# Performance work log

Hardware: AMD Instinct MI355X
Metric: run time of the kernel (lower is better)

The kernel has to match this reference:

```python
import jax, jax.numpy as jnp
import numpy as np

EPS = 1e-8
NUM_ITER = 3
NUM_SLOTS = 8
NUM_HEADS = 4


def _ln(x, w, b):
    m = x.mean(-1, keepdims=True)
    v = x.var(-1, keepdims=True)
    return (x - m) / jnp.sqrt(v + 1e-5) * w + b


def setup_inputs() -> dict:
    key = jax.random.key(0)
    B, T, N, D, S, H = 16, 12, 1024, 256, 128, 256
    K = NUM_SLOTS
    ks = jax.random.split(key, 32)
    w = lambda i, shape: (0.02 * jax.random.normal(ks[i], shape)).astype(jnp.float32)
    f32 = jnp.float32
    return {
        'inputs': jax.random.normal(ks[0], (B, T, N, D), f32),
        'slots_noise': jax.random.normal(ks[1], (B, K, S), f32),
        'slot_mu': w(2, (1, 1, S)),
        'slot_log_sigma': w(3, (1, 1, S)),
        'ln_in_w': jnp.ones((D,), f32), 'ln_in_b': jnp.zeros((D,), f32),
        'ln_slots_w': jnp.ones((S,), f32), 'ln_slots_b': jnp.zeros((S,), f32),
        'ln_mlp_w': jnp.ones((S,), f32), 'ln_mlp_b': jnp.zeros((S,), f32),
        'Wq': w(4, (S, S)), 'Wk': w(5, (D, S)), 'Wv': w(6, (D, S)),
        'gru_Wih': w(7, (3 * S, S)), 'gru_Whh': w(8, (3 * S, S)),
        'gru_bih': jnp.zeros((3 * S,), f32), 'gru_bhh': jnp.zeros((3 * S,), f32),
        'mlp_W1': w(9, (S, H)), 'mlp_b1': jnp.zeros((H,), f32),
        'mlp_W2': w(10, (H, S)), 'mlp_b2': jnp.zeros((S,), f32),
        'p_ln1_w': jnp.ones((S,), f32), 'p_ln1_b': jnp.zeros((S,), f32),
        'p_Wq': w(11, (S, S)), 'p_Wk': w(12, (S, S)), 'p_Wv': w(13, (S, S)), 'p_Wo': w(14, (S, S)),
        'p_ln2_w': jnp.ones((S,), f32), 'p_ln2_b': jnp.zeros((S,), f32),
        'p_ffn_W1': w(15, (S, 4 * S)), 'p_ffn_b1': jnp.zeros((4 * S,), f32),
        'p_ffn_W2': w(16, (4 * S, S)), 'p_ffn_b2': jnp.zeros((S,), f32),
        'p_lnf_w': jnp.ones((S,), f32), 'p_lnf_b': jnp.zeros((S,), f32),
    }


def reference(inputs, slots_noise, slot_mu, slot_log_sigma,
              ln_in_w, ln_in_b, ln_slots_w, ln_slots_b, ln_mlp_w, ln_mlp_b,
              Wq, Wk, Wv, gru_Wih, gru_Whh, gru_bih, gru_bhh,
              mlp_W1, mlp_b1, mlp_W2, mlp_b2,
              p_ln1_w, p_ln1_b, p_Wq, p_Wk, p_Wv, p_Wo,
              p_ln2_w, p_ln2_b, p_ffn_W1, p_ffn_b1, p_ffn_W2, p_ffn_b2,
              p_lnf_w, p_lnf_b):
    B, T, N, D = inputs.shape
    S = slot_mu.shape[-1]
    K = NUM_SLOTS

    slots0 = slot_mu + jnp.exp(slot_log_sigma) * slots_noise  # (B,K,S)
    x = _ln(inputs, ln_in_w, ln_in_b)
    k = (x @ Wk) * (S ** -0.5)  # (B,T,N,S), pre-scaled keys
    v = x @ Wv                  # (B,T,N,S)

    def gru(u, h):  # torch GRUCell semantics; u,h: (B*K,S)
        gi = u @ gru_Wih.T + gru_bih
        gh = h @ gru_Whh.T + gru_bhh
        i_r, i_z, i_n = jnp.split(gi, 3, -1)
        h_r, h_z, h_n = jnp.split(gh, 3, -1)
        r = jax.nn.sigmoid(i_r + h_r)
        z = jax.nn.sigmoid(i_z + h_z)
        n = jnp.tanh(i_n + r * h_n)
        return (1.0 - z) * n + z * h

    def mha(y):  # (B,K,S) self-attention, pre-LN block style
        dh = S // NUM_HEADS
        split = lambda t: t.reshape(B, K, NUM_HEADS, dh).transpose(0, 2, 1, 3)
        q = split(y @ p_Wq) * (dh ** -0.5)
        kk = split(y @ p_Wk)
        vv = split(y @ p_Wv)
        a = jax.nn.softmax(jnp.einsum('bhqd,bhkd->bhqk', q, kk), -1)
        o = jnp.einsum('bhqk,bhkd->bhqd', a, vv).transpose(0, 2, 1, 3).reshape(B, K, S)
        return o @ p_Wo

    def predictor(s):
        s = s + mha(_ln(s, p_ln1_w, p_ln1_b))
        h = _ln(s, p_ln2_w, p_ln2_b)
        s = s + (jax.nn.relu(h @ p_ffn_W1 + p_ffn_b1) @ p_ffn_W2 + p_ffn_b2)
        return _ln(s, p_lnf_w, p_lnf_b)

    def step(slots, kv_t):
        k_t, v_t = kv_t  # (B,N,S) each
        attn_vis = None
        for i in range(NUM_ITER):
            slots_prev = slots
            q = _ln(slots, ln_slots_w, ln_slots_b) @ Wq          # (B,K,S)
            logits = jnp.einsum('bns,bks->bnk', k_t, q)           # (B,N,K)
            attn_vis = jax.nn.softmax(logits, -1)                 # over slots
            attn = attn_vis + EPS
            attn = attn / attn.sum(1, keepdims=True)              # normalize over inputs
            updates = jnp.einsum('bnk,bns->bks', attn, v_t)       # (B,K,S)
            slots = gru(updates.reshape(-1, S), slots_prev.reshape(-1, S)).reshape(B, K, S)
            if i < NUM_ITER - 1:
                h = _ln(slots, ln_mlp_w, ln_mlp_b)
                slots = slots + (jax.nn.relu(h @ mlp_W1 + mlp_b1) @ mlp_W2 + mlp_b2)
        return predictor(slots), (slots, attn_vis)

    kT = jnp.swapaxes(k, 0, 1)  # (T,B,N,S)
    vT = jnp.swapaxes(v, 0, 1)
    _, (slots_seq, attn_seq) = jax.lax.scan(step, slots0, (kT, vT))
    slots_collect = jnp.swapaxes(slots_seq, 0, 1)  # (B,T,K,S)
    attns_collect = jnp.swapaxes(attn_seq, 0, 1)   # (B,T,N,K)
    return slots_collect, attns_collect
```

## Files before the change

kernel.cpp:

```cpp
#include <hip/hip_runtime.h>
#include <hip/hip_bf16.h>

typedef _Float16 half8 __attribute__((ext_vector_type(8)));
typedef float floatx4 __attribute__((ext_vector_type(4)));

#define MFMA_F16(a, b, c) __builtin_amdgcn_mfma_f32_16x16x32_f16((a), (b), (c), 0, 0, 0)

struct PrepJobs {
  const float* src[11];
  _Float16* dst[11];
  int In[11], Out[11], elems[11], doT[11];
  float scale[11];
};

__global__ void prep_all_kernel(PrepJobs J) {
  int j = blockIdx.y;
  int idx = blockIdx.x * 256 + threadIdx.x;
  if (idx >= J.elems[j]) return;
  float v;
  if (J.doT[j]) { int o = idx / J.In[j], i = idx - o * J.In[j]; v = J.src[j][i * J.Out[j] + o]; }
  else          { v = J.src[j][idx]; }
  J.dst[j][idx] = (_Float16)(v * J.scale[j]);
}

__global__ void prep_wtilde_kernel(const float* __restrict__ Wk, const float* __restrict__ Wq,
                                   _Float16* __restrict__ WT, float scale) {
  int idx = blockIdx.x * 256 + threadIdx.x;
  int s = idx >> 8, i = idx & 255;
  const float* wk = Wk + (size_t)i * 128;
  const float* wq = Wq + (size_t)s * 128;
  float acc = 0.f;
  #pragma unroll 4
  for (int o = 0; o < 128; o++) acc += wk[o] * wq[o];
  WT[idx] = (_Float16)(acc * scale);
}

__global__ void init_ctr_kernel(int* __restrict__ ctr) {
  ctr[threadIdx.x] = 0;
}

__global__ __launch_bounds__(256) void gemm_kv_kernel(
    const float* __restrict__ x, const float* __restrict__ lnw_g,
    const float* __restrict__ lnb_g, const _Float16* __restrict__ WT,
    _Float16* __restrict__ kout, _Float16* __restrict__ vTout) {
  __shared__ union {
    struct { _Float16 A[128][72]; _Float16 B[128][72]; } s;
    _Float16 C[128][136];
  } u;
  __shared__ float s_mean[128], s_rstd[128], s_red[256][2], s_lnw[256], s_lnb[256];

  const int tid = threadIdx.x;
  const int bx = blockIdx.x, y = blockIdx.y;
  const size_t r0 = (size_t)bx * 128;
  const int w = tid >> 6, lane = tid & 63, quad = lane >> 4, l15 = lane & 15;

  s_lnw[tid] = lnw_g[tid];
  s_lnb[tid] = lnb_g[tid];
  {
    int row = tid >> 1, half = tid & 1;
    const float* p = x + (r0 + row) * 256 + half * 128;
    float s = 0.f, sq = 0.f;
    for (int i = 0; i < 32; i++) {
      float4 d = ((const float4*)p)[i];
      s += d.x + d.y + d.z + d.w;
      sq += d.x * d.x + d.y * d.y + d.z * d.z + d.w * d.w;
    }
    s_red[tid][0] = s; s_red[tid][1] = sq;
  }
  __syncthreads();
  if (tid < 128) {
    float s  = s_red[2 * tid][0] + s_red[2 * tid + 1][0];
    float sq = s_red[2 * tid][1] + s_red[2 * tid + 1][1];
    float m = s * (1.f / 256.f);
    float v = sq * (1.f / 256.f) - m * m;
    s_mean[tid] = m; s_rstd[tid] = rsqrtf(v + 1e-5f);
  }

  floatx4 acc[2][8];
  for (int rt = 0; rt < 2; rt++)
    for (int ct = 0; ct < 8; ct++) acc[rt][ct] = (floatx4){0.f, 0.f, 0.f, 0.f};

  for (int c = 0; c < 4; c++) {
    __syncthreads();
    for (int i = 0; i < 4; i++) {
      int g = tid + 256 * i;
      int row = g >> 3, c8 = g & 7;
      int col0 = c * 64 + c8 * 8;
      const float* p = x + (r0 + row) * 256 + col0;
      float4 d0 = ((const float4*)p)[0];
      float4 d1 = ((const float4*)p)[1];
      float f[8] = {d0.x, d0.y, d0.z, d0.w, d1.x, d1.y, d1.z, d1.w};
      float m = s_mean[row], rs = s_rstd[row];
      half8 hv;
      #pragma unroll
      for (int j = 0; j < 8; j++)
        hv[j] = (_Float16)((f[j] - m) * rs * s_lnw[col0 + j] + s_lnb[col0 + j]);
      *(half8*)&u.s.A[row][c8 * 8] = hv;
      *(half8*)&u.s.B[row][c8 * 8] = *(const half8*)(WT + (size_t)(y * 128 + row) * 256 + col0);
    }
    __syncthreads();
    #pragma unroll
    for (int ks = 0; ks < 2; ks++) {
      half8 af[2];
      af[0] = *(const half8*)&u.s.A[(2 * w) * 16 + l15][ks * 32 + quad * 8];
      af[1] = *(const half8*)&u.s.A[(2 * w + 1) * 16 + l15][ks * 32 + quad * 8];
      #pragma unroll
      for (int ct = 0; ct < 8; ct++) {
        half8 bf = *(const half8*)&u.s.B[ct * 16 + l15][ks * 32 + quad * 8];
        acc[0][ct] = MFMA_F16(af[0], bf, acc[0][ct]);
        acc[1][ct] = MFMA_F16(af[1], bf, acc[1][ct]);
      }
    }
  }

  const size_t bt = (size_t)(bx >> 3);
  const int n0loc = (bx & 7) * 128;
  if (y == 0) {
    for (int rt = 0; rt < 2; rt++)
      for (int ct = 0; ct < 8; ct++)
        #pragma unroll
        for (int r = 0; r < 4; r++) {
          size_t row = r0 + (2 * w + rt) * 16 + quad * 4 + r;
          kout[row * 128 + ct * 16 + l15] = (_Float16)acc[rt][ct][r];
        }
  } else {
    __syncthreads();
    for (int rt = 0; rt < 2; rt++)
      for (int ct = 0; ct < 8; ct++)
        #pragma unroll
        for (int r = 0; r < 4; r++)
          u.C[(2 * w + rt) * 16 + quad * 4 + r][ct * 16 + l15] = (_Float16)acc[rt][ct][r];
    __syncthreads();
    int s = tid >> 1, hf = tid & 1;
    for (int j = 0; j < 8; j++) {
      int nb = hf * 64 + j * 8;
      half8 tmp;
      #pragma unroll
      for (int e = 0; e < 8; e++) tmp[e] = u.C[nb + e][s];
      *(half8*)(vTout + (bt * 128 + s) * 1024 + n0loc + nb) = tmp;
    }
  }
}

struct P2Args {
  const _Float16 *kbuf, *vT;
  const _Float16 *Wih, *Whh, *W1T, *W2T;
  const _Float16 *pQT, *pKT, *pVT, *pOT, *pF1T, *pF2T;
  const float *noise, *mu, *lsig;
  const float *lnsw, *lnsb, *lnmw, *lnmb;
  const float *bih, *bhh, *mb1, *mb2;
  const float *pl1w, *pl1b, *pl2w, *pl2b, *fb1, *fb2, *plfw, *plfb;
  float *out_slots, *out_attn;
  float *upd_p;
  float *col_p;
  int   *ctr;
};

struct SH {
  _Float16 k_lds[128][136];
  _Float16 v_lds[128][136];
  float slots[8][128];
  _Float16 a16[16][136];
  _Float16 h16[16][136];
  float gh[8][384];
  union {
    struct { _Float16 attnT[16][136]; float wcs[16][8]; } sa;
    struct { _Float16 m16[16][264]; } mlp;
    struct { float qh[8][128]; float kh[8][128]; float vh[8][128]; float sc[4][8][8]; } mha;
    struct { _Float16 f16[16][520]; } ffn;
  } u;
  float bih[384], bhh[384], mb1[256], mb2[128], fb1[512], fb2[128];
  float lnsw[128], lnsb[128], lnmw[128], lnmb[128];
  float pl1w[128], pl1b[128], pl2w[128], pl2b[128], plfw[128], plfb[128];
};

__device__ __forceinline__ void group_barrier(int* ctr, int target) {
  __syncthreads();
  if (threadIdx.x == 0) {
    __hip_atomic_fetch_add(ctr, 1, __ATOMIC_ACQ_REL, __HIP_MEMORY_SCOPE_AGENT);
    while (__hip_atomic_load(ctr, __ATOMIC_ACQUIRE, __HIP_MEMORY_SCOPE_AGENT) < target)
      __builtin_amdgcn_s_sleep(1);
  }
  __syncthreads();
}

__device__ __forceinline__ void ln_to_a16(SH* sh, const float (*src)[128],
                                          const float* wv, const float* bv,
                                          int w, int lane) {
  if (w < 8) {
    float x0 = src[w][lane], x1 = src[w][lane + 64];
    float s = x0 + x1, sq = x0 * x0 + x1 * x1;
    #pragma unroll
    for (int m = 1; m < 64; m <<= 1) { s += __shfl_xor(s, m); sq += __shfl_xor(sq, m); }
    float mn = s * 0.0078125f;
    float vr = sq * 0.0078125f - mn * mn;
    float rs = rsqrtf(vr + 1e-5f);
    sh->a16[w][lane]      = (_Float16)((x0 - mn) * rs * wv[lane]      + bv[lane]);
    sh->a16[w][lane + 64] = (_Float16)((x1 - mn) * rs * wv[lane + 64] + bv[lane + 64]);
  }
}

__global__ __launch_bounds__(1024, 4) void slot_attn_kernel(P2Args P) {
  __shared__ SH sh;
  const int tid = threadIdx.x;
  const int w = tid >> 6, lane = tid & 63, quad = lane >> 4, l15 = lane & 15;
  const int b = blockIdx.x & 15;
  const int g = blockIdx.x >> 4;
  const int n0 = g * 128;
  int* ctrb = P.ctr + b * 64;
  int bar_phase = 0;

  for (int i = tid; i < 384; i += 1024) { sh.bih[i] = P.bih[i]; sh.bhh[i] = P.bhh[i]; }
  for (int i = tid; i < 256; i += 1024) sh.mb1[i] = P.mb1[i];
  for (int i = tid; i < 512; i += 1024) sh.fb1[i] = P.fb1[i];
  if (tid < 128) {
    sh.mb2[tid]  = P.mb2[tid];  sh.fb2[tid]  = P.fb2[tid];
    sh.lnsw[tid] = P.lnsw[tid]; sh.lnsb[tid] = P.lnsb[tid];
    sh.lnmw[tid] = P.lnmw[tid]; sh.lnmb[tid] = P.lnmb[tid];
    sh.pl1w[tid] = P.pl1w[tid]; sh.pl1b[tid] = P.pl1b[tid];
    sh.pl2w[tid] = P.pl2w[tid]; sh.pl2b[tid] = P.pl2b[tid];
    sh.plfw[tid] = P.plfw[tid]; sh.plfb[tid] = P.plfb[tid];
  }
  {
    int kk = tid >> 7, s = tid & 127;
    float v = P.mu[s] + expf(P.lsig[s]) * P.noise[(b * 8 + kk) * 128 + s];
    sh.slots[kk][s] = v;
    sh.h16[kk][s] = (_Float16)v;
  }
  if (w >= 8) {
    sh.a16[w][lane] = (_Float16)0.f; sh.a16[w][lane + 64] = (_Float16)0.f;
    sh.h16[w][lane] = (_Float16)0.f; sh.h16[w][lane + 64] = (_Float16)0.f;
  }
  __syncthreads();

  for (int t = 0; t < 12; t++) {
    const _Float16* kt = P.kbuf + ((size_t)(b * 12 + t)) * 1024 * 128 + (size_t)n0 * 128;
    const _Float16* vt = P.vT   + ((size_t)(b * 12 + t)) * 128 * 1024 + n0;
    {
      int r = tid >> 4, c8 = (tid & 15) * 8;
      #pragma unroll
      for (int p = 0; p < 2; p++) {
        int row = p * 64 + r;
        *(half8*)&sh.k_lds[row][c8] = *(const half8*)(kt + (size_t)row * 128 + c8);
        *(half8*)&sh.v_lds[row][c8] = *(const half8*)(vt + (size_t)row * 1024 + c8);
      }
    }
    __syncthreads();

    for (int it = 0; it < 3; it++) {
      const int par = (t * 3 + it) & 1;
      float* updg = P.upd_p + ((size_t)(par * 16 + b) * 8 + g) * 1152;
      float* colg = P.col_p + ((size_t)(par * 16 + b) * 8 + g) * 64;
      if (w < 8) {
        float x0 = sh.slots[w][lane], x1 = sh.slots[w][lane + 64];
        float s = x0 + x1, sq = x0 * x0 + x1 * x1;
        #pragma unroll
        for (int m = 1; m < 64; m <<= 1) { s += __shfl_xor(s, m); sq += __shfl_xor(sq, m); }
        float mn = s * 0.0078125f;
        float vr = sq * 0.0078125f - mn * mn;
        float rs = rsqrtf(vr + 1e-5f);
        sh.a16[w][lane]      = (_Float16)((x0 - mn) * rs * sh.lnsw[lane]      + sh.lnsb[lane]);
        sh.a16[w][lane + 64] = (_Float16)((x1 - mn) * rs * sh.lnsw[lane + 64] + sh.lnsb[lane + 64]);
      } else {
        const int idx8 = w - 8;
        const _Float16* ar = &sh.h16[l15][quad * 8];
        #pragma unroll
        for (int tt = 0; tt < 3; tt++) {
          int ct = idx8 + tt * 8;
          const _Float16* Bg = P.Whh + (size_t)(ct * 16 + l15) * 128 + quad * 8;
          floatx4 acc = (floatx4){0.f, 0.f, 0.f, 0.f};
          #pragma unroll
          for (int ks = 0; ks < 4; ks++)
            acc = MFMA_F16(*(const half8*)(ar + ks * 32), *(const half8*)(Bg + ks * 32), acc);
          int col = ct * 16 + l15;
          #pragma unroll
          for (int r = 0; r < 4; r++) {
            int slot = quad * 4 + r;
            if (slot < 8) sh.gh[slot][col] = acc[r] + sh.bhh[col];
          }
        }
      }
      __syncthreads();
      {
        int nloc0 = (w & 7) * 16;
        int rhalf = w >> 3;
        floatx4 acc = (floatx4){0.f, 0.f, 0.f, 0.f};
        const _Float16* ar = &sh.k_lds[nloc0 + l15][quad * 8];
        const _Float16* br = &sh.a16[l15][quad * 8];
        #pragma unroll
        for (int ks = 0; ks < 4; ks++)
          acc = MFMA_F16(*(const half8*)(ar + ks * 32), *(const half8*)(br + ks * 32), acc);
        float cs = 0.f;
        #pragma unroll
        for (int rr = 0; rr < 2; rr++) {
          int r = rhalf * 2 + rr;
          float v = (l15 < 8) ? acc[r] : -3.0e38f;
          float mx = v;
          mx = fmaxf(mx, __shfl_xor(mx, 1, 16));
          mx = fmaxf(mx, __shfl_xor(mx, 2, 16));
          mx = fmaxf(mx, __shfl_xor(mx, 4, 16));
          mx = fmaxf(mx, __shfl_xor(mx, 8, 16));
          float pv = (l15 < 8) ? expf(v - mx) : 0.f;
          float ss = pv;
          ss += __shfl_xor(ss, 1, 16); ss += __shfl_xor(ss, 2, 16);
          ss += __shfl_xor(ss, 4, 16); ss += __shfl_xor(ss, 8, 16);
          float pn = pv / ss;
          cs += pn;
          int nloc = nloc0 + quad * 4 + r;
          sh.u.sa.attnT[l15][nloc] = (l15 == 8) ? (_Float16)1.f : (_Float16)pn;
          if (it == 2 && l15 < 8)
            P.out_attn[((size_t)(b * 12 + t) * 1024 + n0 + nloc) * 8 + l15] = pn;
        }
        cs += __shfl_xor(cs, 16); cs += __shfl_xor(cs, 32);
        if (lane < 8) sh.u.sa.wcs[w][lane] = cs;
      }
      __syncthreads();
      if (w < 8) {
        floatx4 acc = (floatx4){0.f, 0.f, 0.f, 0.f};
        const _Float16* ar = &sh.u.sa.attnT[l15][quad * 8];
        const _Float16* br = &sh.v_lds[w * 16 + l15][quad * 8];
        #pragma unroll
        for (int ks = 0; ks < 4; ks++)
          acc = MFMA_F16(*(const half8*)(ar + ks * 32), *(const half8*)(br + ks * 32), acc);
        int scol = w * 16 + l15;
        #pragma unroll
        for (int r = 0; r < 4; r++) {
          int row = quad * 4 + r;
          if (row < 9)
            __hip_atomic_store(&updg[row * 128 + scol], acc[r],
                               __ATOMIC_RELAXED, __HIP_MEMORY_SCOPE_AGENT);
        }
      }
      if (tid < 8) {
        float c = 0.f;
        #pragma unroll
        for (int ww = 0; ww < 16; ww++) c += sh.u.sa.wcs[ww][tid];
        __hip_atomic_store(&colg[tid], c, __ATOMIC_RELAXED, __HIP_MEMORY_SCOPE_AGENT);
      }
      bar_phase++;
      group_barrier(ctrb, 8 * bar_phase);
      {
        int slot = tid >> 7, scol = tid & 127;
        const float* upb = P.upd_p + (size_t)(par * 16 + b) * 8 * 1152;
        float sum = 0.f, vs = 0.f;
        #pragma unroll
        for (int gg = 0; gg < 8; gg++) {
          sum += __hip_atomic_load((float*)(upb + gg * 1152 + slot * 128 + scol),
                                   __ATOMIC_RELAXED, __HIP_MEMORY_SCOPE_AGENT);
          vs  += __hip_atomic_load((float*)(upb + gg * 1152 + 8 * 128 + scol),
                                   __ATOMIC_RELAXED, __HIP_MEMORY_SCOPE_AGENT);
        }
        const float* cpb = P.col_p + (size_t)(par * 16 + b) * 8 * 64;
        float csum = 0.f;
        #pragma unroll
        for (int gg = 0; gg < 8; gg++)
          csum += __hip_atomic_load((float*)(cpb + gg * 64 + slot),
                                    __ATOMIC_RELAXED, __HIP_MEMORY_SCOPE_AGENT);
        float upd = (sum + 1e-8f * vs) / (csum + 1024.f * 1e-8f);
        sh.a16[slot][scol] = (_Float16)upd;
      }
      __syncthreads();
      if (w < 8) {
        const _Float16* ar = &sh.a16[l15][quad * 8];
        const _Float16* B0 = P.Wih + (size_t)(w * 16 + l15) * 128 + quad * 8;
        const _Float16* B1 = P.Wih + (size_t)((w + 8) * 16 + l15) * 128 + quad * 8;
        const _Float16* B2 = P.Wih + (size_t)((w + 16) * 16 + l15) * 128 + quad * 8;
        floatx4 ac = (floatx4){0.f, 0.f, 0.f, 0.f};
        floatx4 az = (floatx4){0.f, 0.f, 0.f, 0.f};
        floatx4 an = (floatx4){0.f, 0.f, 0.f, 0.f};
        #pragma unroll
        for (int ks = 0; ks < 4; ks++) {
          half8 af = *(const half8*)(ar + ks * 32);
          ac = MFMA_F16(af, *(const half8*)(B0 + ks * 32), ac);
          az = MFMA_F16(af, *(const half8*)(B1 + ks * 32), az);
          an = MFMA_F16(af, *(const half8*)(B2 + ks * 32), an);
        }
        int col = w * 16 + l15;
        #pragma unroll
        for (int r = 0; r < 4; r++) {
          int slot = quad * 4 + r;
          if (slot < 8) {
            float gic = ac[r] + sh.bih[col];
            float giz = az[r] + sh.bih[128 + col];
            float gin = an[r] + sh.bih[256 + col];
            float rg = 1.f / (1.f + expf(-(gic + sh.gh[slot][col])));
            float zg = 1.f / (1.f + expf(-(giz + sh.gh[slot][128 + col])));
            float ng = tanhf(gin + rg * sh.gh[slot][256 + col]);
            float h = sh.slots[slot][col];
            float x = (1.f - zg) * ng + zg * h;
            sh.slots[slot][col] = x;
            if (it == 2)
              P.out_slots[((size_t)(b * 12 + t) * 8 + slot) * 128 + col] = x;
          }
        }
      }
      __syncthreads();
      ln_to_a16(&sh, sh.slots, (it < 2) ? sh.lnmw : sh.pl1w,
                (it < 2) ? sh.lnmb : sh.pl1b, w, lane);
      __syncthreads();
      if (it < 2) {
        {
          floatx4 acc = (floatx4){0.f, 0.f, 0.f, 0.f};
          const _Float16* ar = &sh.a16[l15][quad * 8];
          const _Float16* br = P.W1T + (size_t)(w * 16 + l15) * 128 + quad * 8;
          #pragma unroll
          for (int ks = 0; ks < 4; ks++)
            acc = MFMA_F16(*(const half8*)(ar + ks * 32), *(const half8*)(br + ks * 32), acc);
          int col = w * 16 + l15;
          #pragma unroll
          for (int r = 0; r < 4; r++) {
            int slot = quad * 4 + r;
            if (slot < 8) sh.u.mlp.m16[slot][col] = (_Float16)fmaxf(acc[r] + sh.mb1[col], 0.f);
            else          sh.u.mlp.m16[slot][col] = (_Float16)0.f;
          }
        }
        __syncthreads();
        if (w < 8) {
          floatx4 acc = (floatx4){0.f, 0.f, 0.f, 0.f};
          const _Float16* ar = &sh.u.mlp.m16[l15][quad * 8];
          const _Float16* br = P.W2T + (size_t)(w * 16 + l15) * 256 + quad * 8;
          #pragma unroll
          for (int ks = 0; ks < 8; ks++)
            acc = MFMA_F16(*(const half8*)(ar + ks * 32), *(const half8*)(br + ks * 32), acc);
          int col = w * 16 + l15;
          #pragma unroll
          for (int r = 0; r < 4; r++) {
            int slot = quad * 4 + r;
            if (slot < 8) {
              float ns = sh.slots[slot][col] + acc[r] + sh.mb2[col];
              sh.slots[slot][col] = ns;
              sh.h16[slot][col] = (_Float16)ns;
            }
          }
        }
        __syncthreads();
      }
    }

    {
      const _Float16* ar = &sh.a16[l15][quad * 8];
      int gg = w >> 3, ct = w & 7, col = ct * 16 + l15;
      const _Float16* Bg = (gg == 0 ? P.pQT : P.pKT) + (size_t)(ct * 16 + l15) * 128 + quad * 8;
      floatx4 acc = (floatx4){0.f, 0.f, 0.f, 0.f};
      #pragma unroll
      for (int ks = 0; ks < 4; ks++)
        acc = MFMA_F16(*(const half8*)(ar + ks * 32), *(const half8*)(Bg + ks * 32), acc);
      float scale = (gg == 0) ? 0.17677669529663687f : 1.f;
      float* dst = (gg == 0) ? &sh.u.mha.qh[0][0] : &sh.u.mha.kh[0][0];
      #pragma unroll
      for (int r = 0; r < 4; r++) {
        int slot = quad * 4 + r;
        if (slot < 8) dst[slot * 128 + col] = acc[r] * scale;
      }
      if (w < 8) {
        const _Float16* Bg2 = P.pVT + (size_t)(w * 16 + l15) * 128 + quad * 8;
        floatx4 a2 = (floatx4){0.f, 0.f, 0.f, 0.f};
        #pragma unroll
        for (int ks = 0; ks < 4; ks++)
          a2 = MFMA_F16(*(const half8*)(ar + ks * 32), *(const half8*)(Bg2 + ks * 32), a2);
        int colv = w * 16 + l15;
        #pragma unroll
        for (int r = 0; r < 4; r++) {
          int slot = quad * 4 + r;
          if (slot < 8) sh.u.mha.vh[slot][colv] = a2[r];
        }
      }
    }
    __syncthreads();
    if (w < 4) {
      int h = w, a = lane >> 3, b2 = lane & 7;
      const float* qr = &sh.u.mha.qh[a][h * 32];
      const float* kr = &sh.u.mha.kh[b2][h * 32];
      float s = 0.f;
      #pragma unroll
      for (int d = 0; d < 32; d++) s += qr[d] * kr[d];
      float mx = s;
      mx = fmaxf(mx, __shfl_xor(mx, 1, 8));
      mx = fmaxf(mx, __shfl_xor(mx, 2, 8));
      mx = fmaxf(mx, __shfl_xor(mx, 4, 8));
      float e = expf(s - mx);
      float ssum = e;
      ssum += __shfl_xor(ssum, 1, 8); ssum += __shfl_xor(ssum, 2, 8); ssum += __shfl_xor(ssum, 4, 8);
      float p = e / ssum;
      float o0 = 0.f, o1 = 0.f, o2 = 0.f, o3 = 0.f;
      int d0 = h * 32 + b2 * 4;
      #pragma unroll
      for (int j = 0; j < 8; j++) {
        float pj = __shfl(p, (a << 3) + j);
        const float* vr = &sh.u.mha.vh[j][d0];
        o0 += pj * vr[0]; o1 += pj * vr[1]; o2 += pj * vr[2]; o3 += pj * vr[3];
      }
      sh.a16[a][d0]     = (_Float16)o0;
      sh.a16[a][d0 + 1] = (_Float16)o1;
      sh.a16[a][d0 + 2] = (_Float16)o2;
      sh.a16[a][d0 + 3] = (_Float16)o3;
    }
    __syncthreads();
    if (w < 8) {
      floatx4 acc = (floatx4){0.f, 0.f, 0.f, 0.f};
      const _Float16* ar = &sh.a16[l15][quad * 8];
      const _Float16* br = P.pOT + (size_t)(w * 16 + l15) * 128 + quad * 8;
      #pragma unroll
      for (int ks = 0; ks < 4; ks++)
        acc = MFMA_F16(*(const half8*)(ar + ks * 32), *(const half8*)(br + ks * 32), acc);
      int col = w * 16 + l15;
      #pragma unroll
      for (int r = 0; r < 4; r++) {
        int slot = quad * 4 + r;
        if (slot < 8) sh.slots[slot][col] += acc[r];
      }
    }
    __syncthreads();
    ln_to_a16(&sh, sh.slots, sh.pl2w, sh.pl2b, w, lane);
    __syncthreads();
    for (int ct = w; ct < 32; ct += 16) {
      floatx4 acc = (floatx4){0.f, 0.f, 0.f, 0.f};
      const _Float16* ar = &sh.a16[l15][quad * 8];
      const _Float16* br = P.pF1T + (size_t)(ct * 16 + l15) * 128 + quad * 8;
      #pragma unroll
      for (int ks = 0; ks < 4; ks++)
        acc = MFMA_F16(*(const half8*)(ar + ks * 32), *(const half8*)(br + ks * 32), acc);
      int col = ct * 16 + l15;
      #pragma unroll
      for (int r = 0; r < 4; r++) {
        int slot = quad * 4 + r;
        if (slot < 8) sh.u.ffn.f16[slot][col] = (_Float16)fmaxf(acc[r] + sh.fb1[col], 0.f);
        else          sh.u.ffn.f16[slot][col] = (_Float16)0.f;
      }
    }
    __syncthreads();
    if (w < 8) {
      floatx4 acc = (floatx4){0.f, 0.f, 0.f, 0.f};
      const _Float16* ar = &sh.u.ffn.f16[l15][quad * 8];
      const _Float16* br = P.pF2T + (size_t)(w * 16 + l15) * 512 + quad * 8;
      #pragma unroll 4
      for (int ks = 0; ks < 16; ks++)
        acc = MFMA_F16(*(const half8*)(ar + ks * 32), *(const half8*)(br + ks * 32), acc);
      int col = w * 16 + l15;
      #pragma unroll
      for (int r = 0; r < 4; r++) {
        int slot = quad * 4 + r;
        if (slot < 8) sh.slots[slot][col] += acc[r] + sh.fb2[col];
      }
    }
    __syncthreads();
    if (w < 8) {
      float x0 = sh.slots[w][lane], x1 = sh.slots[w][lane + 64];
      float s = x0 + x1, sq = x0 * x0 + x1 * x1;
      #pragma unroll
      for (int m = 1; m < 64; m <<= 1) { s += __shfl_xor(s, m); sq += __shfl_xor(sq, m); }
      float mn = s * 0.0078125f;
      float vr = sq * 0.0078125f - mn * mn;
      float rs = rsqrtf(vr + 1e-5f);
      float y0 = (x0 - mn) * rs * sh.plfw[lane]      + sh.plfb[lane];
      float y1 = (x1 - mn) * rs * sh.plfw[lane + 64] + sh.plfb[lane + 64];
      sh.slots[w][lane] = y0;      sh.slots[w][lane + 64] = y1;
      sh.h16[w][lane] = (_Float16)y0; sh.h16[w][lane + 64] = (_Float16)y1;
    }
    __syncthreads();
  }
}

extern "C" void kernel_launch(void* const* d_in, const int* in_sizes, int n_in,
                              void* d_out, int out_size, void* d_ws, size_t ws_size,
                              hipStream_t stream) {
  const float* inp   = (const float*)d_in[0];
  const float* noise = (const float*)d_in[1];
  const float* mu    = (const float*)d_in[2];
  const float* lsig  = (const float*)d_in[3];
  const float* lniw  = (const float*)d_in[4];
  const float* lnib  = (const float*)d_in[5];
  const float* lnsw  = (const float*)d_in[6];
  const float* lnsb  = (const float*)d_in[7];
  const float* lnmw  = (const float*)d_in[8];
  const float* lnmb  = (const float*)d_in[9];
  const float* Wq    = (const float*)d_in[10];
  const float* Wk    = (const float*)d_in[11];
  const float* Wv    = (const float*)d_in[12];
  const float* gWih  = (const float*)d_in[13];
  const float* gWhh  = (const float*)d_in[14];
  const float* gbih  = (const float*)d_in[15];
  const float* gbhh  = (const float*)d_in[16];
  const float* mW1   = (const float*)d_in[17];
  const float* mb1   = (const float*)d_in[18];
  const float* mW2   = (const float*)d_in[19];
  const float* mb2   = (const float*)d_in[20];
  const float* pl1w  = (const float*)d_in[21];
  const float* pl1b  = (const float*)d_in[22];
  const float* pWq   = (const float*)d_in[23];
  const float* pWk   = (const float*)d_in[24];
  const float* pWv   = (const float*)d_in[25];
  const float* pWo   = (const float*)d_in[26];
  const float* pl2w  = (const float*)d_in[27];
  const float* pl2b  = (const float*)d_in[28];
  const float* pf1   = (const float*)d_in[29];
  const float* pfb1  = (const float*)d_in[30];
  const float* pf2   = (const float*)d_in[31];
  const float* pfb2  = (const float*)d_in[32];
  const float* plfw  = (const float*)d_in[33];
  const float* plfb  = (const float*)d_in[34];

  _Float16* p   = (_Float16*)d_ws;
  _Float16* kbuf = p;  p += 25165824;
  _Float16* vT   = p;  p += 25165824;
  _Float16* WT   = p;  p += 65536;
  _Float16* Wih  = p;  p += 49152;
  _Float16* Whh  = p;  p += 49152;
  _Float16* W1T  = p;  p += 32768;
  _Float16* W2T  = p;  p += 32768;
  _Float16* pQT  = p;  p += 16384;
  _Float16* pKT  = p;  p += 16384;
  _Float16* pVT  = p;  p += 16384;
  _Float16* pOT  = p;  p += 16384;
  _Float16* pF1T = p;  p += 65536;
  _Float16* pF2T = p;  p += 65536;
  float* fb   = (float*)p;
  float* upd_p = fb;  fb += 2 * 16 * 8 * 1152;
  float* col_p = fb;  fb += 2 * 16 * 8 * 64;
  int*   ctr   = (int*)fb;

  const float kscale = 0.08838834764831845f;
  init_ctr_kernel<<<1, 1024, 0, stream>>>(ctr);

  PrepJobs J;
  const float* srcs[11] = {Wv, gWih, gWhh, mW1, mW2, pWq, pWk, pWv, pWo, pf1, pf2};
  _Float16* dsts[11]    = {WT + 32768, Wih, Whh, W1T, W2T, pQT, pKT, pVT, pOT, pF1T, pF2T};
  int Ins[11]    = {256, 49152, 49152, 128, 256, 128, 128, 128, 128, 128, 512};
  int Outs[11]   = {128, 1, 1, 256, 128, 128, 128, 128, 128, 512, 128};
  int elemss[11] = {32768, 49152, 49152, 32768, 32768, 16384, 16384, 16384, 16384, 65536, 65536};
  int doTs[11]   = {1, 0, 0, 1, 1, 1, 1, 1, 1, 1, 1};
  float scales[11] = {1.f, 1.f, 1.f, 1.f, 1.f, 1.f, 1.f, 1.f, 1.f, 1.f, 1.f};
  for (int j = 0; j < 11; j++) {
    J.src[j] = srcs[j]; J.dst[j] = dsts[j]; J.In[j] = Ins[j]; J.Out[j] = Outs[j];
    J.elems[j] = elemss[j]; J.doT[j] = doTs[j]; J.scale[j] = scales[j];
  }
  dim3 gp(256, 11, 1);
  prep_all_kernel<<<gp, 256, 0, stream>>>(J);
  prep_wtilde_kernel<<<128, 256, 0, stream>>>(Wk, Wq, WT, kscale);

  dim3 g1(1536, 2, 1);
  gemm_kv_kernel<<<g1, 256, 0, stream>>>(inp, lniw, lnib, WT, kbuf, vT);

  P2Args a;
  a.kbuf = kbuf; a.vT = vT;
  a.Wih = Wih; a.Whh = Whh; a.W1T = W1T; a.W2T = W2T;
  a.pQT = pQT; a.pKT = pKT; a.pVT = pVT; a.pOT = pOT; a.pF1T = pF1T; a.pF2T = pF2T;
  a.noise = noise; a.mu = mu; a.lsig = lsig;
  a.lnsw = lnsw; a.lnsb = lnsb; a.lnmw = lnmw; a.lnmb = lnmb;
  a.bih = gbih; a.bhh = gbhh; a.mb1 = mb1; a.mb2 = mb2;
  a.pl1w = pl1w; a.pl1b = pl1b; a.pl2w = pl2w; a.pl2b = pl2b;
  a.fb1 = pfb1; a.fb2 = pfb2; a.plfw = plfw; a.plfb = plfb;
  a.out_slots = (float*)d_out;
  a.out_attn  = (float*)d_out + 196608;
  a.upd_p = upd_p; a.col_p = col_p; a.ctr = ctr;

  slot_attn_kernel<<<128, 1024, 0, stream>>>(a);
}
```

Baseline: 1.389 ms.

## Spread GRU input projection across all waves and fuse gate update with LayerNorm

The GRU input-gate matmul now runs on all 16 waves, with the third gate block on waves 0-7, and writes gi to a new shared buffer. A separate pass of 8 waves, one slot row each, then applies the gates and immediately computes the following LayerNorm via shuffles, which removes the separate ln_to_a16 call and one barrier. The epsilon-weighted v column sum is now loaded only on the first iteration and reused, since V is unchanged within a timestep. The change adds 12KB of LDS and an extra barrier, which could lower occupancy.

New measurement: 1.325 ms. 4.6% less time.

```diff
diff --git a/kernel.cpp b/kernel.cpp
--- a/kernel.cpp
+++ b/kernel.cpp
@@ -162,6 +162,7 @@
   float slots[8][128];
   _Float16 a16[16][136];
   _Float16 h16[16][136];
+  float gi[8][384];
   float gh[8][384];
   union {
     struct { _Float16 attnT[16][136]; float wcs[16][8]; } sa;
@@ -246,6 +247,8 @@
       }
     }
     __syncthreads();
+
+    float vsv = 0.f;
 
     for (int it = 0; it < 3; it++) {
       const int par = (t * 3 + it) & 1;
@@ -342,61 +345,84 @@
       {
         int slot = tid >> 7, scol = tid & 127;
         const float* upb = P.upd_p + (size_t)(par * 16 + b) * 8 * 1152;
-        float sum = 0.f, vs = 0.f;
-        #pragma unroll
-        for (int gg = 0; gg < 8; gg++) {
+        float sum = 0.f;
+        #pragma unroll
+        for (int gg = 0; gg < 8; gg++)
           sum += __hip_atomic_load((float*)(upb + gg * 1152 + slot * 128 + scol),
                                    __ATOMIC_RELAXED, __HIP_MEMORY_SCOPE_AGENT);
-          vs  += __hip_atomic_load((float*)(upb + gg * 1152 + 8 * 128 + scol),
-                                   __ATOMIC_RELAXED, __HIP_MEMORY_SCOPE_AGENT);
-        }
         const float* cpb = P.col_p + (size_t)(par * 16 + b) * 8 * 64;
         float csum = 0.f;
         #pragma unroll
         for (int gg = 0; gg < 8; gg++)
           csum += __hip_atomic_load((float*)(cpb + gg * 64 + slot),
                                     __ATOMIC_RELAXED, __HIP_MEMORY_SCOPE_AGENT);
-        float upd = (sum + 1e-8f * vs) / (csum + 1024.f * 1e-8f);
+        if (it == 0) {
+          float vs = 0.f;
+          #pragma unroll
+          for (int gg = 0; gg < 8; gg++)
+            vs += __hip_atomic_load((float*)(upb + gg * 1152 + 8 * 128 + scol),
+                                    __ATOMIC_RELAXED, __HIP_MEMORY_SCOPE_AGENT);
+          vsv = vs;
+        }
+        float upd = (sum + 1e-8f * vsv) / (csum + 1024.f * 1e-8f);
         sh.a16[slot][scol] = (_Float16)upd;
+      }
+      __syncthreads();
+      {
+        const _Float16* ar = &sh.a16[l15][quad * 8];
+        const _Float16* Bg = P.Wih + (size_t)(w * 16 + l15) * 128 + quad * 8;
+        floatx4 acc = (floatx4){0.f, 0.f, 0.f, 0.f};
+        #pragma unroll
+        for (int ks = 0; ks < 4; ks++)
+          acc = MFMA_F16(*(const half8*)(ar + ks * 32), *(const half8*)(Bg + ks * 32), acc);
+        int col = w * 16 + l15;
+        #pragma unroll
+        for (int r = 0; r < 4; r++) {
+          int slot = quad * 4 + r;
+          if (slot < 8) sh.gi[slot][col] = acc[r] + sh.bih[col];
+        }
+        if (w < 8) {
+          int col2 = (16 + w) * 16 + l15;
+          const _Float16* Bg2 = P.Wih + (size_t)((16 + w) * 16 + l15) * 128 + quad * 8;
+          floatx4 acc2 = (floatx4){0.f, 0.f, 0.f, 0.f};
+          #pragma unroll
+          for (int ks = 0; ks < 4; ks++)
+            acc2 = MFMA_F16(*(const half8*)(ar + ks * 32), *(const half8*)(Bg2 + ks * 32), acc2);
+          #pragma unroll
+          for (int r = 0; r < 4; r++) {
+            int slot = quad * 4 + r;
+            if (slot < 8) sh.gi[slot][col2] = acc2[r] + sh.bih[col2];
+          }
+        }
       }
       __syncthreads();
       if (w < 8) {
-        const _Float16* ar = &sh.a16[l15][quad * 8];
-        const _Float16* B0 = P.Wih + (size_t)(w * 16 + l15) * 128 + quad * 8;
-        const _Float16* B1 = P.Wih + (size_t)((w + 8) * 16 + l15) * 128 + quad * 8;
-        const _Float16* B2 = P.Wih + (size_t)((w + 16) * 16 + l15) * 128 + quad * 8;
-        floatx4 ac = (floatx4){0.f, 0.f, 0.f, 0.f};
-        floatx4 az = (floatx4){0.f, 0.f, 0.f, 0.f};
-        floatx4 an = (floatx4){0.f, 0.f, 0.f, 0.f};
-        #pragma unroll
-        for (int ks = 0; ks < 4; ks++) {
-          half8 af = *(const half8*)(ar + ks * 32);
-          ac = MFMA_F16(af, *(const half8*)(B0 + ks * 32), ac);
-          az = MFMA_F16(af, *(const half8*)(B1 + ks * 32), az);
-          an = MFMA_F16(af, *(const half8*)(B2 + ks * 32), an);
-        }
-        int col = w * 16 + l15;
-        #pragma unroll
-        for (int r = 0; r < 4; r++) {
-          int slot = quad * 4 + r;
-          if (slot < 8) {
-            float gic = ac[r] + sh.bih[col];
-            float giz = az[r] + sh.bih[128 + col];
-            float gin = an[r] + sh.bih[256 + col];
-            float rg = 1.f / (1.f + expf(-(gic + sh.gh[slot][col])));
-            float zg = 1.f / (1.f + expf(-(giz + sh.gh[slot][128 + col])));
-            float ng = tanhf(gin + rg * sh.gh[slot][256 + col]);
-            float h = sh.slots[slot][col];
-            float x = (1.f - zg) * ng + zg * h;
-            sh.slots[slot][col] = x;
-            if (it == 2)
-              P.out_slots[((size_t)(b * 12 + t) * 8 + slot) * 128 + col] = x;
-          }
-        }
-      }
-      __syncthreads();
-      ln_to_a16(&sh, sh.slots, (it < 2) ? sh.lnmw : sh.pl1w,
-                (it < 2) ? sh.lnmb : sh.pl1b, w, lane);
+        float h0 = sh.slots[w][lane], h1 = sh.slots[w][lane + 64];
+        float r0 = 1.f / (1.f + expf(-(sh.gi[w][lane]       + sh.gh[w][lane])));
+        float z0 = 1.f / (1.f + expf(-(sh.gi[w][128 + lane] + sh.gh[w][128 + lane])));
+        float n0v = tanhf(sh.gi[w][256 + lane] + r0 * sh.gh[w][256 + lane]);
+        float x0 = (1.f - z0) * n0v + z0 * h0;
+        int l64 = lane + 64;
+        float r1 = 1.f / (1.f + expf(-(sh.gi[w][l64]       + sh.gh[w][l64])));
+        float z1 = 1.f / (1.f + expf(-(sh.gi[w][128 + l64] + sh.gh[w][128 + l64])));
+        float n1v = tanhf(sh.gi[w][256 + l64] + r1 * sh.gh[w][256 + l64]);
+        float x1 = (1.f - z1) * n1v + z1 * h1;
+        sh.slots[w][lane] = x0; sh.slots[w][lane + 64] = x1;
+        if (it == 2 && g == 0) {
+          P.out_slots[((size_t)(b * 12 + t) * 8 + w) * 128 + lane]      = x0;
+          P.out_slots[((size_t)(b * 12 + t) * 8 + w) * 128 + lane + 64] = x1;
+        }
+        const float* wv = (it < 2) ? sh.lnmw : sh.pl1w;
+        const float* bv = (it < 2) ? sh.lnmb : sh.pl1b;
+        float s = x0 + x1, sq = x0 * x0 + x1 * x1;
+        #pragma unroll
+        for (int m = 1; m < 64; m <<= 1) { s += __shfl_xor(s, m); sq += __shfl_xor(sq, m); }
+        float mn = s * 0.0078125f;
+        float vr = sq * 0.0078125f - mn * mn;
+        float rs = rsqrtf(vr + 1e-5f);
+        sh.a16[w][lane]      = (_Float16)((x0 - mn) * rs * wv[lane]      + bv[lane]);
+        sh.a16[w][lane + 64] = (_Float16)((x1 - mn) * rs * wv[lane + 64] + bv[lane + 64]);
+      }
       __syncthreads();
       if (it < 2) {
         {
```
